# Kernel tuning notes

Measured on AMD Instinct MI355X. Metric: run time of the kernel, lower is better.

## Reference

```python
import jax, jax.numpy as jnp
import numpy as np

H = 8          # attention heads
EPS = 1e-5     # LayerNorm eps (torch default)
B, T, E = 8, 1024, 128
D, DI, N, DC, R = 512, 1024, 16, 4, 32   # d_model, d_inner, d_state, d_conv, dt_rank
NT, NM = 6, 8                            # transformer layers, mamba layers
FF = 2048                                # transformer dim_feedforward (torch default)


def setup_inputs():
    key = jax.random.key(0)
    ks = iter(jax.random.split(key, 48))
    def rn(shape, scale=0.05):
        return jax.random.normal(next(ks), shape, jnp.float32) * scale
    return {
        "emb":      jax.random.normal(next(ks), (B, T, E), jnp.float32),
        # TransformerEncoder (6 post-norm layers), params stacked on leading layer dim
        "t_wqkv":   rn((NT, 3 * E, E)), "t_bqkv": jnp.zeros((NT, 3 * E), jnp.float32),
        "t_wo":     rn((NT, E, E)),     "t_bo":   jnp.zeros((NT, E), jnp.float32),
        "t_ln1w":   jnp.ones((NT, E), jnp.float32),  "t_ln1b": jnp.zeros((NT, E), jnp.float32),
        "t_w1":     rn((NT, FF, E)),    "t_b1":   jnp.zeros((NT, FF), jnp.float32),
        "t_w2":     rn((NT, E, FF)),    "t_b2":   jnp.zeros((NT, E), jnp.float32),
        "t_ln2w":   jnp.ones((NT, E), jnp.float32),  "t_ln2b": jnp.zeros((NT, E), jnp.float32),
        # Linear(emb_dim -> d_model)
        "w_in":     rn((D, E)), "b_in": jnp.zeros((D,), jnp.float32),
        # MambaBlocks (8 raw Mamba layers, no residual/norm), stacked
        "m_inproj": rn((NM, 2 * DI, D)),
        "m_convw":  rn((NM, DI, DC), 0.2), "m_convb": jnp.zeros((NM, DI), jnp.float32),
        "m_xproj":  rn((NM, R + 2 * N, DI)),
        "m_dtw":    rn((NM, DI, R), 0.1),
        "m_dtb":    jax.random.uniform(next(ks), (NM, DI), jnp.float32, -6.0, -3.0),
        "m_Alog":   jnp.log(jnp.tile(jnp.arange(1, N + 1, dtype=jnp.float32), (NM, DI, 1))),
        "m_D":      jnp.ones((NM, DI), jnp.float32),
        "m_outproj": rn((NM, D, DI)),
        # Linear(d_model -> emb_dim)
        "w_out":    rn((E, D)), "b_out": jnp.zeros((E,), jnp.float32),
    }


def _ln(x, w, b):
    mu = jnp.mean(x, -1, keepdims=True)
    var = jnp.var(x, -1, keepdims=True)
    return (x - mu) * jax.lax.rsqrt(var + EPS) * w + b


def _tlayer(x, p):
    wqkv, bqkv, wo, bo, ln1w, ln1b, w1, b1, w2, b2, ln2w, ln2b = p
    qkv = x @ wqkv.T + bqkv                        # (B,T,3E)
    q, k, v = jnp.split(qkv, 3, axis=-1)
    def heads(t):                                  # (B,T,E) -> (B,H,T,E//H)
        return t.reshape(B, T, H, E // H).transpose(0, 2, 1, 3)
    q, k, v = heads(q), heads(k), heads(v)
    scores = jnp.einsum("bhqd,bhkd->bhqk", q, k) / jnp.sqrt(jnp.float32(E // H))
    attn = jax.nn.softmax(scores, axis=-1)
    o = jnp.einsum("bhqk,bhkd->bhqd", attn, v).transpose(0, 2, 1, 3).reshape(B, T, E)
    x = _ln(x + o @ wo.T + bo, ln1w, ln1b)         # post-norm (torch default)
    ff = jax.nn.relu(x @ w1.T + b1) @ w2.T + b2
    return _ln(x + ff, ln2w, ln2b)


def _mamba_layer(x, p):
    inproj, convw, convb, xproj, dtw, dtb, Alog, Dp, outproj = p
    xz = x @ inproj.T                              # (B,T,2*DI)
    xi, z = jnp.split(xz, 2, axis=-1)
    # causal depthwise conv1d, kernel DC, left-padded
    xp = jnp.pad(xi, ((0, 0), (DC - 1, 0), (0, 0)))
    conv = sum(xp[:, k:k + T, :] * convw[:, k] for k in range(DC)) + convb
    xi = jax.nn.silu(conv)
    dbc = xi @ xproj.T                             # (B,T,R+2N)
    dt_r, Bt, Ct = dbc[..., :R], dbc[..., R:R + N], dbc[..., R + N:]
    dt = jax.nn.softplus(dt_r @ dtw.T + dtb)       # (B,T,DI)
    A = -jnp.exp(Alog)                             # (DI,N)
    def step(h, inputs):
        dt_t, B_t, C_t, x_t = inputs               # (B,DI),(B,N),(B,N),(B,DI)
        dA = jnp.exp(dt_t[:, :, None] * A)         # (B,DI,N)
        h = h * dA + (dt_t * x_t)[:, :, None] * B_t[:, None, :]
        y = jnp.einsum("bdn,bn->bd", h, C_t)
        return h, y
    h0 = jnp.zeros((B, DI, N), x.dtype)
    seq = (dt.transpose(1, 0, 2), Bt.transpose(1, 0, 2),
           Ct.transpose(1, 0, 2), xi.transpose(1, 0, 2))
    _, ys = jax.lax.scan(step, h0, seq)            # ys: (T,B,DI)
    y = ys.transpose(1, 0, 2) + Dp * xi
    y = y * jax.nn.silu(z)
    return y @ outproj.T                           # (B,T,D)


def reference(emb, t_wqkv, t_bqkv, t_wo, t_bo, t_ln1w, t_ln1b, t_w1, t_b1, t_w2, t_b2,
              t_ln2w, t_ln2b, w_in, b_in, m_inproj, m_convw, m_convb, m_xproj, m_dtw,
              m_dtb, m_Alog, m_D, m_outproj, w_out, b_out):
    x = emb
    tparams = (t_wqkv, t_bqkv, t_wo, t_bo, t_ln1w, t_ln1b, t_w1, t_b1, t_w2, t_b2, t_ln2w, t_ln2b)
    for i in range(NT):
        x = _tlayer(x, tuple(p[i] for p in tparams))
    x = x @ w_in.T + b_in                          # (B,T,D)
    mparams = (m_inproj, m_convw, m_convb, m_xproj, m_dtw, m_dtb, m_Alog, m_D, m_outproj)
    for i in range(NM):
        x = _mamba_layer(x, tuple(p[i] for p in mparams))
    return x @ w_out.T + b_out                     # (B,T,E)
```

## Files before the change

### kernel.cpp

```cpp
#include <hip/hip_runtime.h>
#include <math.h>

#define HB 8
#define TT 1024
#define NSTATE 16
#define NTT 6
#define NMM 8
#define MM (HB*TT)
#define EPSV 1e-5f
#define CHUNK 64
#define NCH (TT/CHUNK)
#define LSTR 72
#define AKS 128
#define VSTR 132

typedef _Float16 f16x8 __attribute__((ext_vector_type(8)));
typedef _Float16 f16x4 __attribute__((ext_vector_type(4)));
typedef float f32x4_t __attribute__((ext_vector_type(4)));

static __device__ inline void split8(const float4 a, const float4 b,
                                     f16x8& h, f16x8& l)
{
  float x[8] = {a.x, a.y, a.z, a.w, b.x, b.y, b.z, b.w};
#pragma unroll
  for (int i = 0; i < 8; i++) {
    _Float16 hi = (_Float16)x[i];
    h[i] = hi;
    l[i] = (_Float16)(x[i] - (float)hi);
  }
}

template<int TN>
__global__ __launch_bounds__(256) void gemm_mfma_t(
    const float* __restrict__ A, int lda,
    const float* __restrict__ W,
    const float* __restrict__ bias,
    float* __restrict__ C,
    float* __restrict__ P,
    int N, int K, int S, int act)
{
  __shared__ _Float16 As[128 * LSTR];
  __shared__ _Float16 Bs[TN * LSTR];
  const int tid = threadIdx.x;
  const int m0 = blockIdx.y * 128;
  const int n0 = blockIdx.x * TN;
  const int z = blockIdx.z;
  const int kchunk = K / S;
  const int kb = z * kchunk;
  const int ke = kb + kchunk;

  const int lr = tid >> 1;
  const int lh = tid & 1;
  const int lane = tid & 63;
  const int w = tid >> 6;
  const int quad = lane >> 4;
  const int l16 = lane & 15;

  const float* Arow = A + (size_t)(m0 + lr) * lda + lh * 16;
  _Float16* Adst = &As[lr * LSTR + lh * 16];

  constexpr int MI = (TN == 128) ? 4 : 2;
  const int w0 = (TN == 128) ? (w & 1) : w;
  const int w1 = (TN == 128) ? (w >> 1) : 0;
  const int rowbase = (TN == 128) ? w0 * 64 : w0 * 32;

  f32x4_t acc[MI][4];
#pragma unroll
  for (int i = 0; i < MI; i++)
#pragma unroll
    for (int j = 0; j < 4; j++)
#pragma unroll
      for (int r = 0; r < 4; r++) acc[i][j][r] = 0.f;

  const _Float16* ab = &As[(rowbase + l16) * LSTR + quad * 8];
  const _Float16* bb = &Bs[(w1 * 64 + l16) * LSTR + quad * 8];

  const float* Wrow;
  _Float16* Bdst;
  if (TN == 128) {
    Wrow = W + (size_t)(n0 + lr) * K + lh * 16;
    Bdst = &Bs[lr * LSTR + lh * 16];
  } else {
    const int br = tid >> 2;
    const int bo = (tid & 3) * 8;
    Wrow = W + (size_t)(n0 + br) * K + bo;
    Bdst = &Bs[br * LSTR + bo];
  }

  for (int k0 = kb; k0 < ke; k0 += 32) {
    float4 a0 = *(const float4*)&Arow[k0];
    float4 a1 = *(const float4*)&Arow[k0 + 4];
    float4 a2 = *(const float4*)&Arow[k0 + 8];
    float4 a3 = *(const float4*)&Arow[k0 + 12];
    float4 b0 = *(const float4*)&Wrow[k0];
    float4 b1 = *(const float4*)&Wrow[k0 + 4];
    float4 b2, b3;
    if (TN == 128) {
      b2 = *(const float4*)&Wrow[k0 + 8];
      b3 = *(const float4*)&Wrow[k0 + 12];
    }
    __syncthreads();
    {
      f16x8 h, l;
      split8(a0, a1, h, l);
      *(f16x8*)&Adst[0] = h; *(f16x8*)&Adst[32] = l;
      split8(a2, a3, h, l);
      *(f16x8*)&Adst[8] = h; *(f16x8*)&Adst[40] = l;
      split8(b0, b1, h, l);
      *(f16x8*)&Bdst[0] = h; *(f16x8*)&Bdst[32] = l;
      if (TN == 128) {
        split8(b2, b3, h, l);
        *(f16x8*)&Bdst[8] = h; *(f16x8*)&Bdst[40] = l;
      }
    }
    __syncthreads();

    f16x8 bh[4], bl[4];
#pragma unroll
    for (int ni = 0; ni < 4; ni++) {
      bh[ni] = *(const f16x8*)&bb[ni * 16 * LSTR];
      bl[ni] = *(const f16x8*)&bb[ni * 16 * LSTR + 32];
    }
#pragma unroll
    for (int mi = 0; mi < MI; mi++) {
      f16x8 ah = *(const f16x8*)&ab[mi * 16 * LSTR];
      f16x8 al = *(const f16x8*)&ab[mi * 16 * LSTR + 32];
#pragma unroll
      for (int ni = 0; ni < 4; ni++) {
        acc[mi][ni] = __builtin_amdgcn_mfma_f32_16x16x32_f16(ah, bh[ni], acc[mi][ni], 0, 0, 0);
        acc[mi][ni] = __builtin_amdgcn_mfma_f32_16x16x32_f16(ah, bl[ni], acc[mi][ni], 0, 0, 0);
        acc[mi][ni] = __builtin_amdgcn_mfma_f32_16x16x32_f16(al, bh[ni], acc[mi][ni], 0, 0, 0);
      }
    }
  }

  float* dst = (S == 1) ? C : (P + (size_t)z * MM * N);
#pragma unroll
  for (int ni = 0; ni < 4; ni++) {
    const int n = n0 + w1 * 64 + ni * 16 + l16;
    const float bv = (S == 1 && bias) ? bias[n] : 0.f;
#pragma unroll
    for (int mi = 0; mi < MI; mi++) {
      const int mbase = m0 + rowbase + mi * 16 + quad * 4;
#pragma unroll
      for (int r = 0; r < 4; r++) {
        float v = acc[mi][ni][r] + bv;
        if (S == 1) {
          if (act == 1) v = fmaxf(v, 0.f);
          else if (act == 2) v = fmaxf(v, 0.f) + log1pf(__expf(-fabsf(v)));
        }
        dst[(size_t)(mbase + r) * N + n] = v;
      }
    }
  }
}

__global__ __launch_bounds__(256) void reduce_k(
    const float* __restrict__ P, const float* __restrict__ bias,
    float* __restrict__ C, int nmask, int S, int act, int stride4)
{
  const int idx = blockIdx.x * 256 + threadIdx.x;
  float4 a = *(const float4*)&P[(size_t)idx * 4];
  for (int z = 1; z < S; z++) {
    float4 p = *(const float4*)&P[(size_t)(idx + z * (size_t)stride4) * 4];
    a.x += p.x; a.y += p.y; a.z += p.z; a.w += p.w;
  }
  if (bias) {
    float4 bv = *(const float4*)&bias[(idx * 4) & nmask];
    a.x += bv.x; a.y += bv.y; a.z += bv.z; a.w += bv.w;
  }
  if (act == 1) {
    a.x = fmaxf(a.x, 0.f); a.y = fmaxf(a.y, 0.f);
    a.z = fmaxf(a.z, 0.f); a.w = fmaxf(a.w, 0.f);
  } else if (act == 2) {
    a.x = fmaxf(a.x, 0.f) + log1pf(__expf(-fabsf(a.x)));
    a.y = fmaxf(a.y, 0.f) + log1pf(__expf(-fabsf(a.y)));
    a.z = fmaxf(a.z, 0.f) + log1pf(__expf(-fabsf(a.z)));
    a.w = fmaxf(a.w, 0.f) + log1pf(__expf(-fabsf(a.w)));
  }
  *(float4*)&C[(size_t)idx * 4] = a;
}

__global__ __launch_bounds__(256) void attn_mfma_k(
    const float* __restrict__ qkv, float* __restrict__ o)
{
  __shared__ _Float16 Khi[AKS * 16], Klo[AKS * 16];
  __shared__ _Float16 Vthi[16 * VSTR], Vtlo[16 * VSTR];
  __shared__ float Pscr[4][16 * 18];

  const int tid = threadIdx.x;
  const int lane = tid & 63;
  const int wv = tid >> 6;
  const int quad = lane >> 4;
  const int l16 = lane & 15;
  const int qh = quad & 1;
  const int bh = blockIdx.y;
  const int b = bh >> 3;
  const int h = bh & 7;
  const int qb0 = blockIdx.x * 128;

  f16x8 qa[2];
#pragma unroll
  for (int u = 0; u < 2; u++) {
    const int qrow = qb0 + wv * 32 + u * 16 + l16;
    const float* qp = qkv + (size_t)(b * TT + qrow) * 384 + h * 16 + qh * 8;
    float4 x0 = *(const float4*)&qp[0];
    float4 x1 = *(const float4*)&qp[4];
    float xv[8] = {x0.x, x0.y, x0.z, x0.w, x1.x, x1.y, x1.z, x1.w};
#pragma unroll
    for (int j = 0; j < 8; j++) {
      float q = xv[j] * 0.25f;
      _Float16 hi = (_Float16)q;
      _Float16 lo = (_Float16)(q - (float)hi);
      qa[u][j] = (quad < 2) ? hi : lo;
    }
  }

  f32x4_t oacc[2];
  float lacc[2][4];
#pragma unroll
  for (int u = 0; u < 2; u++)
#pragma unroll
    for (int r = 0; r < 4; r++) { oacc[u][r] = 0.f; lacc[u][r] = 0.f; }

  float* Pw = &Pscr[wv][0];

  for (int ks = 0; ks < TT; ks += AKS) {
    __syncthreads();
    {
      const int key = tid >> 1, hf = tid & 1;
      const float* kp = qkv + (size_t)(b * TT + ks + key) * 384 + 128 + h * 16 + hf * 8;
      float4 k0 = *(const float4*)&kp[0];
      float4 k1 = *(const float4*)&kp[4];
      f16x8 vh, vl;
      split8(k0, k1, vh, vl);
      *(f16x8*)&Khi[key * 16 + hf * 8] = vh;
      *(f16x8*)&Klo[key * 16 + hf * 8] = vl;
      const float* vp = kp + 128;
      float4 v0 = *(const float4*)&vp[0];
      float4 v1 = *(const float4*)&vp[4];
      float vvv[8] = {v0.x, v0.y, v0.z, v0.w, v1.x, v1.y, v1.z, v1.w};
#pragma unroll
      for (int j = 0; j < 8; j++) {
        const int d = hf * 8 + j;
        _Float16 hi = (_Float16)vvv[j];
        Vthi[d * VSTR + key] = hi;
        Vtlo[d * VSTR + key] = (_Float16)(vvv[j] - (float)hi);
      }
    }
    __syncthreads();

    for (int kt = 0; kt < AKS; kt += 16) {
      f16x8 kfh = *(const f16x8*)&Khi[(kt + l16) * 16 + qh * 8];
      f16x8 kfl = *(const f16x8*)&Klo[(kt + l16) * 16 + qh * 8];
      const int vo = l16 * VSTR + kt + qh * 8;
      f16x4 va0 = *(const f16x4*)&Vthi[vo];
      f16x4 va1 = *(const f16x4*)&Vthi[vo + 4];
      f16x4 vb0 = *(const f16x4*)&Vtlo[vo];
      f16x4 vb1 = *(const f16x4*)&Vtlo[vo + 4];
      f16x8 vfh, vfl;
#pragma unroll
      for (int i = 0; i < 4; i++) {
        vfh[i] = va0[i]; vfh[4 + i] = va1[i];
        vfl[i] = vb0[i]; vfl[4 + i] = vb1[i];
      }

#pragma unroll
      for (int u = 0; u < 2; u++) {
        f32x4_t s;
#pragma unroll
        for (int r = 0; r < 4; r++) s[r] = 0.f;
        s = __builtin_amdgcn_mfma_f32_16x16x32_f16(qa[u], kfh, s, 0, 0, 0);
        s = __builtin_amdgcn_mfma_f32_16x16x32_f16(qa[u], kfl, s, 0, 0, 0);
        float p[4];
#pragma unroll
        for (int r = 0; r < 4; r++) {
          p[r] = __expf(s[r]);
          lacc[u][r] += p[r];
        }
        float* ps = Pw + (quad * 4) * 18 + l16;
        ps[0] = p[0]; ps[18] = p[1]; ps[36] = p[2]; ps[54] = p[3];
        __asm__ volatile("s_waitcnt lgkmcnt(0)" ::: "memory");
        const float* pr = Pw + l16 * 18 + qh * 8;
        f16x8 pa;
#pragma unroll
        for (int j = 0; j < 8; j++) {
          float pv = pr[j];
          _Float16 hi = (_Float16)pv;
          _Float16 lo = (_Float16)(pv - (float)hi);
          pa[j] = (quad < 2) ? hi : lo;
        }
        oacc[u] = __builtin_amdgcn_mfma_f32_16x16x32_f16(pa, vfh, oacc[u], 0, 0, 0);
        oacc[u] = __builtin_amdgcn_mfma_f32_16x16x32_f16(pa, vfl, oacc[u], 0, 0, 0);
        __asm__ volatile("s_waitcnt lgkmcnt(0)" ::: "memory");
      }
    }
  }

#pragma unroll
  for (int u = 0; u < 2; u++) {
#pragma unroll
    for (int r = 0; r < 4; r++) {
      float lv = lacc[u][r];
      lv += __shfl_xor(lv, 1);
      lv += __shfl_xor(lv, 2);
      lv += __shfl_xor(lv, 4);
      lv += __shfl_xor(lv, 8);
      const float inv = 1.f / lv;
      const int qrow = qb0 + wv * 32 + u * 16 + quad * 4 + r;
      o[(size_t)(b * TT + qrow) * 128 + h * 16 + l16] = oacc[u][r] * inv;
    }
  }
}

__global__ __launch_bounds__(256) void add_ln_k(
    const float* __restrict__ a, const float* __restrict__ bvec,
    const float* __restrict__ w, const float* __restrict__ bb,
    float* __restrict__ out)
{
  const int tid = threadIdx.x;
  const int wave = tid >> 6, lane = tid & 63;
  const size_t row = (size_t)blockIdx.x * 4 + wave;
  const float* pa = a + row * 128;
  const float* pb = bvec + row * 128;
  float v0 = pa[lane] + pb[lane];
  float v1 = pa[lane + 64] + pb[lane + 64];
  float s1 = v0 + v1, s2 = v0 * v0 + v1 * v1;
#pragma unroll
  for (int off = 32; off; off >>= 1) {
    s1 += __shfl_down(s1, off);
    s2 += __shfl_down(s2, off);
  }
  s1 = __shfl(s1, 0); s2 = __shfl(s2, 0);
  const float mean = s1 * (1.f / 128.f);
  const float var = s2 * (1.f / 128.f) - mean * mean;
  const float rs = rsqrtf(var + EPSV);
  out[row * 128 + lane]      = (v0 - mean) * rs * w[lane] + bb[lane];
  out[row * 128 + lane + 64] = (v1 - mean) * rs * w[lane + 64] + bb[lane + 64];
}

__global__ __launch_bounds__(256) void conv_silu_k(
    const float* __restrict__ xz, const float* __restrict__ cw,
    const float* __restrict__ cb, float* __restrict__ out)
{
  const int idx = blockIdx.x * 256 + threadIdx.x;
  const int di = idx & 1023;
  const int m = idx >> 10;
  const int t = m & (TT - 1);
  float acc = cb[di];
#pragma unroll
  for (int k = 0; k < 4; k++) {
    int tt = t + k - 3;
    if (tt >= 0) acc += xz[(size_t)(m + k - 3) * 2048 + di] * cw[di * 4 + k];
  }
  out[(size_t)m * 1024 + di] = acc / (1.f + __expf(-acc));
}

__global__ __launch_bounds__(64) void scan_partial_k(
    const float* __restrict__ dt,
    const float* __restrict__ dbc,
    const float* __restrict__ xi,
    const float* __restrict__ Alog,
    float* __restrict__ Pb, float* __restrict__ Sb)
{
  const int slice = blockIdx.x & 15;
  const int c = blockIdx.x >> 4;
  const int b = blockIdx.y;
  const int di = slice * 64 + threadIdx.x;

  float A[NSTATE];
#pragma unroll
  for (int n = 0; n < NSTATE; n++) A[n] = -__expf(Alog[di * NSTATE + n]);
  float h[NSTATE], P[NSTATE];
#pragma unroll
  for (int n = 0; n < NSTATE; n++) { h[n] = 0.f; P[n] = 1.f; }

  const size_t m0 = (size_t)b * TT + (size_t)c * CHUNK;
  for (int t = 0; t < CHUNK; t++) {
    const size_t m = m0 + t;
    const float dtv = dt[m * 1024 + di];
    const float xv  = xi[m * 1024 + di];
    const float dtx = dtv * xv;
#pragma unroll
    for (int n = 0; n < NSTATE; n++) {
      const float Bv = dbc[m * 64 + 32 + n];
      const float dA = __expf(dtv * A[n]);
      h[n] = h[n] * dA + dtx * Bv;
      P[n] *= dA;
    }
  }
  const size_t base = (((size_t)b * NCH + c) * NSTATE) * 1024 + di;
#pragma unroll
  for (int n = 0; n < NSTATE; n++) {
    Pb[base + (size_t)n * 1024] = P[n];
    Sb[base + (size_t)n * 1024] = h[n];
  }
}

__global__ __launch_bounds__(256) void scan_fix_k(
    float* __restrict__ Pb, const float* __restrict__ Sb)
{
  const int idx = blockIdx.x * 256 + threadIdx.x;
  const int b = idx >> 10;
  const int di = idx & 1023;
  float h[NSTATE];
#pragma unroll
  for (int n = 0; n < NSTATE; n++) h[n] = 0.f;
  for (int c = 0; c < NCH; c++) {
    const size_t base = (((size_t)b * NCH + c) * NSTATE) * 1024 + di;
    float P[NSTATE], S[NSTATE];
#pragma unroll
    for (int n = 0; n < NSTATE; n++) {
      P[n] = Pb[base + (size_t)n * 1024];
      S[n] = Sb[base + (size_t)n * 1024];
    }
#pragma unroll
    for (int n = 0; n < NSTATE; n++) {
      Pb[base + (size_t)n * 1024] = h[n];
      h[n] = P[n] * h[n] + S[n];
    }
  }
}

__global__ __launch_bounds__(64) void scan_final_k(
    const float* __restrict__ dt,
    const float* __restrict__ dbc,
    const float* __restrict__ xi,
    const float* __restrict__ xz,
    const float* __restrict__ Alog,
    const float* __restrict__ Dp,
    const float* __restrict__ Hin,
    float* __restrict__ Y)
{
  const int slice = blockIdx.x & 15;
  const int c = blockIdx.x >> 4;
  const int b = blockIdx.y;
  const int di = slice * 64 + threadIdx.x;

  float A[NSTATE];
#pragma unroll
  for (int n = 0; n < NSTATE; n++) A[n] = -__expf(Alog[di * NSTATE + n]);
  const float Dv = Dp[di];
  float h[NSTATE];
  const size_t hbase = (((size_t)b * NCH + c) * NSTATE) * 1024 + di;
#pragma unroll
  for (int n = 0; n < NSTATE; n++) h[n] = Hin[hbase + (size_t)n * 1024];

  const size_t m0 = (size_t)b * TT + (size_t)c * CHUNK;
  for (int t = 0; t < CHUNK; t++) {
    const size_t m = m0 + t;
    const float dtv = dt[m * 1024 + di];
    const float xv  = xi[m * 1024 + di];
    const float zv  = xz[m * 2048 + 1024 + di];
    const float dtx = dtv * xv;
    float y = 0.f;
#pragma unroll
    for (int n = 0; n < NSTATE; n++) {
      const float Bv = dbc[m * 64 + 32 + n];
      const float Cv = dbc[m * 64 + 48 + n];
      const float dA = __expf(dtv * A[n]);
      h[n] = h[n] * dA + dtx * Bv;
      y += h[n] * Cv;
    }
    y += Dv * xv;
    y *= zv / (1.f + __expf(-zv));
    Y[m * 1024 + di] = y;
  }
}

extern "C" void kernel_launch(void* const* d_in, const int* in_sizes, int n_in,
                              void* d_out, int out_size, void* d_ws, size_t ws_size,
                              hipStream_t stream)
{
  const float* emb      = (const float*)d_in[0];
  const float* t_wqkv   = (const float*)d_in[1];
  const float* t_bqkv   = (const float*)d_in[2];
  const float* t_wo     = (const float*)d_in[3];
  const float* t_bo     = (const float*)d_in[4];
  const float* t_ln1w   = (const float*)d_in[5];
  const float* t_ln1b   = (const float*)d_in[6];
  const float* t_w1     = (const float*)d_in[7];
  const float* t_b1     = (const float*)d_in[8];
  const float* t_w2     = (const float*)d_in[9];
  const float* t_b2     = (const float*)d_in[10];
  const float* t_ln2w   = (const float*)d_in[11];
  const float* t_ln2b   = (const float*)d_in[12];
  const float* w_in     = (const float*)d_in[13];
  const float* b_in     = (const float*)d_in[14];
  const float* m_inproj = (const float*)d_in[15];
  const float* m_convw  = (const float*)d_in[16];
  const float* m_convb  = (const float*)d_in[17];
  const float* m_xproj  = (const float*)d_in[18];
  const float* m_dtw    = (const float*)d_in[19];
  const float* m_dtb    = (const float*)d_in[20];
  const float* m_Alog   = (const float*)d_in[21];
  const float* m_D      = (const float*)d_in[22];
  const float* m_outproj= (const float*)d_in[23];
  const float* w_out    = (const float*)d_in[24];
  const float* b_out    = (const float*)d_in[25];

  float* ws = (float*)d_ws;
  float* X0   = ws;
  float* X1   = X0 + (size_t)MM * 512;
  float* Abuf = X1 + (size_t)MM * 512;
  float* Bf   = Abuf + (size_t)MM * 2048;
  float* Cf   = Bf + (size_t)MM * 1024;
  float* Yb   = Cf + (size_t)MM * 1024;
  float* Db   = Yb + (size_t)MM * 1024;

  dim3 blk(256);
  auto gemm = [&](const float* A, int lda, const float* W, const float* bias,
                  float* C, int N, int K, int act, int S, float* P, bool tn64) {
    dim3 g(N / (tn64 ? 64 : 128), MM / 128, S);
    if (tn64)
      hipLaunchKernelGGL(gemm_mfma_t<64>, g, blk, 0, stream,
                         A, lda, W, S == 1 ? bias : nullptr, C, P, N, K, S, act);
    else
      hipLaunchKernelGGL(gemm_mfma_t<128>, g, blk, 0, stream,
                         A, lda, W, S == 1 ? bias : nullptr, C, P, N, K, S, act);
    if (S > 1) {
      int stride4 = (MM * N) / 4;
      hipLaunchKernelGGL(reduce_k, dim3(stride4 / 256), blk, 0, stream,
                         P, bias, C, N - 1, S, act, stride4);
    }
  };

  const float* x = emb;
  for (int l = 0; l < NTT; l++) {
    gemm(x, 128, t_wqkv + (size_t)l * 384 * 128, t_bqkv + l * 384,
         Abuf, 384, 128, 0, 1, nullptr, false);
    hipLaunchKernelGGL(attn_mfma_k, dim3(TT / 128, HB * 8), blk, 0, stream,
                       Abuf, Yb);
    gemm(Yb, 128, t_wo + (size_t)l * 128 * 128, t_bo + l * 128,
         Cf, 128, 128, 0, 2, X1, true);
    hipLaunchKernelGGL(add_ln_k, dim3(MM / 4), blk, 0, stream,
                       x, Cf, t_ln1w + l * 128, t_ln1b + l * 128, X0);
    gemm(X0, 128, t_w1 + (size_t)l * 2048 * 128, t_b1 + l * 2048,
         Abuf, 2048, 128, 1, 1, nullptr, false);
    gemm(Abuf, 2048, t_w2 + (size_t)l * 128 * 2048, t_b2 + l * 128,
         Cf, 128, 2048, 0, 8, Yb, false);
    hipLaunchKernelGGL(add_ln_k, dim3(MM / 4), blk, 0, stream,
                       X0, Cf, t_ln2w + l * 128, t_ln2b + l * 128, X0);
    x = X0;
  }

  gemm(X0, 128, w_in, b_in, X1, 512, 128, 0, 1, nullptr, false);

  float* xc = X1;
  float* xo = X0;
  for (int l = 0; l < NMM; l++) {
    gemm(xc, 512, m_inproj + (size_t)l * 2048 * 512, nullptr,
         Abuf, 2048, 512, 0, 1, nullptr, false);
    hipLaunchKernelGGL(conv_silu_k, dim3(MM * 1024 / 256), blk, 0, stream,
                       Abuf, m_convw + (size_t)l * 1024 * 4, m_convb + l * 1024, Bf);
    gemm(Bf, 1024, m_xproj + (size_t)l * 64 * 1024, nullptr,
         Db, 64, 1024, 0, 4, xo, true);
    gemm(Db, 64, m_dtw + (size_t)l * 1024 * 32, m_dtb + l * 1024,
         Cf, 1024, 32, 2, 1, nullptr, false);

    float* Pb = xo;
    float* Sb = xo + (size_t)HB * NCH * NSTATE * 1024;
    hipLaunchKernelGGL(scan_partial_k, dim3(16 * NCH, HB), dim3(64), 0, stream,
                       Cf, Db, Bf, m_Alog + (size_t)l * 1024 * 16, Pb, Sb);
    hipLaunchKernelGGL(scan_fix_k, dim3(MM / 1024 * 4), blk, 0, stream, Pb, Sb);
    hipLaunchKernelGGL(scan_final_k, dim3(16 * NCH, HB), dim3(64), 0, stream,
                       Cf, Db, Bf, Abuf,
                       m_Alog + (size_t)l * 1024 * 16, m_D + l * 1024, Pb, Yb);

    gemm(Yb, 1024, m_outproj + (size_t)l * 512 * 1024, nullptr,
         xo, 512, 1024, 0, 2, Abuf, false);
    float* tmp = xc; xc = xo; xo = tmp;
  }

  gemm(xc, 512, w_out, b_out, (float*)d_out, 128, 512, 0, 4, Yb, false);
}
```

Before: 3.641 ms.

## Pre-split weights and GEMM activations into fp16 hi/lo planes before MFMA GEMMs

Adds a split kernel that converts fp32 tensors into separate fp16 high and low planes. All weight matrices are split once per forward call, and activations feeding the QKV, FF1, input-projection and Mamba in-projection GEMMs are split just before those GEMMs. The GEMM kernel can then load the pre-split fp16 planes straight into shared memory instead of converting fp32 to hi/lo in every tile, which each block otherwise repeats. The price is extra kernel launches, an extra pass over the split tensors, and a larger workspace. The weight pre-split path runs only when the workspace is big enough.

```diff
diff --git a/kernel.cpp b/kernel.cpp
--- a/kernel.cpp
+++ b/kernel.cpp
@@ -30,10 +30,30 @@
   }
 }
 
+__global__ __launch_bounds__(256) void split_k(
+    const float* __restrict__ X, _Float16* __restrict__ Hi,
+    _Float16* __restrict__ Lo)
+{
+  const size_t i = ((size_t)blockIdx.x * 256 + threadIdx.x) * 4;
+  float4 v = *(const float4*)&X[i];
+  float x[4] = {v.x, v.y, v.z, v.w};
+  f16x4 h, l;
+#pragma unroll
+  for (int j = 0; j < 4; j++) {
+    _Float16 hi = (_Float16)x[j];
+    h[j] = hi;
+    l[j] = (_Float16)(x[j] - (float)hi);
+  }
+  *(f16x4*)&Hi[i] = h;
+  *(f16x4*)&Lo[i] = l;
+}
+
 template<int TN>
 __global__ __launch_bounds__(256) void gemm_mfma_t(
     const float* __restrict__ A, int lda,
     const float* __restrict__ W,
+    const _Float16* __restrict__ Ahi, const _Float16* __restrict__ Alo,
+    const _Float16* __restrict__ Whi, const _Float16* __restrict__ Wlo,
     const float* __restrict__ bias,
     float* __restrict__ C,
     float* __restrict__ P,
@@ -57,6 +77,8 @@
   const int l16 = lane & 15;
 
   const float* Arow = A + (size_t)(m0 + lr) * lda + lh * 16;
+  const _Float16* AHrow = Ahi ? (Ahi + (size_t)(m0 + lr) * lda + lh * 16) : nullptr;
+  const _Float16* ALrow = Ahi ? (Alo + (size_t)(m0 + lr) * lda + lh * 16) : nullptr;
   _Float16* Adst = &As[lr * LSTR + lh * 16];
 
   constexpr int MI = (TN == 128) ? 4 : 2;
@@ -76,36 +98,74 @@
   const _Float16* bb = &Bs[(w1 * 64 + l16) * LSTR + quad * 8];
 
   const float* Wrow;
+  const _Float16* WHrow = nullptr;
+  const _Float16* WLrow = nullptr;
   _Float16* Bdst;
   if (TN == 128) {
     Wrow = W + (size_t)(n0 + lr) * K + lh * 16;
+    if (Whi) {
+      WHrow = Whi + (size_t)(n0 + lr) * K + lh * 16;
+      WLrow = Wlo + (size_t)(n0 + lr) * K + lh * 16;
+    }
     Bdst = &Bs[lr * LSTR + lh * 16];
   } else {
     const int br = tid >> 2;
     const int bo = (tid & 3) * 8;
     Wrow = W + (size_t)(n0 + br) * K + bo;
+    if (Whi) {
+      WHrow = Whi + (size_t)(n0 + br) * K + bo;
+      WLrow = Wlo + (size_t)(n0 + br) * K + bo;
+    }
     Bdst = &Bs[br * LSTR + bo];
   }
 
   for (int k0 = kb; k0 < ke; k0 += 32) {
-    float4 a0 = *(const float4*)&Arow[k0];
-    float4 a1 = *(const float4*)&Arow[k0 + 4];
-    float4 a2 = *(const float4*)&Arow[k0 + 8];
-    float4 a3 = *(const float4*)&Arow[k0 + 12];
-    float4 b0 = *(const float4*)&Wrow[k0];
-    float4 b1 = *(const float4*)&Wrow[k0 + 4];
-    float4 b2, b3;
-    if (TN == 128) {
-      b2 = *(const float4*)&Wrow[k0 + 8];
-      b3 = *(const float4*)&Wrow[k0 + 12];
+    f16x8 ah0, ah1, al0, al1;
+    float4 a0, a1, a2, a3;
+    if (Ahi) {
+      ah0 = *(const f16x8*)&AHrow[k0];
+      ah1 = *(const f16x8*)&AHrow[k0 + 8];
+      al0 = *(const f16x8*)&ALrow[k0];
+      al1 = *(const f16x8*)&ALrow[k0 + 8];
+    } else {
+      a0 = *(const float4*)&Arow[k0];
+      a1 = *(const float4*)&Arow[k0 + 4];
+      a2 = *(const float4*)&Arow[k0 + 8];
+      a3 = *(const float4*)&Arow[k0 + 12];
+    }
+    f16x8 wh0, wh1, wl0, wl1;
+    float4 b0, b1, b2, b3;
+    if (Whi) {
+      wh0 = *(const f16x8*)&WHrow[k0];
+      wl0 = *(const f16x8*)&WLrow[k0];
+      if (TN == 128) {
+        wh1 = *(const f16x8*)&WHrow[k0 + 8];
+        wl1 = *(const f16x8*)&WLrow[k0 + 8];
+      }
+    } else {
+      b0 = *(const float4*)&Wrow[k0];
+      b1 = *(const float4*)&Wrow[k0 + 4];
+      if (TN == 128) {
+        b2 = *(const float4*)&Wrow[k0 + 8];
+        b3 = *(const float4*)&Wrow[k0 + 12];
+      }
     }
     __syncthreads();
-    {
+    if (Ahi) {
+      *(f16x8*)&Adst[0] = ah0; *(f16x8*)&Adst[8] = ah1;
+      *(f16x8*)&Adst[32] = al0; *(f16x8*)&Adst[40] = al1;
+    } else {
       f16x8 h, l;
       split8(a0, a1, h, l);
       *(f16x8*)&Adst[0] = h; *(f16x8*)&Adst[32] = l;
       split8(a2, a3, h, l);
       *(f16x8*)&Adst[8] = h; *(f16x8*)&Adst[40] = l;
+    }
+    if (Whi) {
+      *(f16x8*)&Bdst[0] = wh0; *(f16x8*)&Bdst[32] = wl0;
+      if (TN == 128) { *(f16x8*)&Bdst[8] = wh1; *(f16x8*)&Bdst[40] = wl1; }
+    } else {
+      f16x8 h, l;
       split8(b0, b1, h, l);
       *(f16x8*)&Bdst[0] = h; *(f16x8*)&Bdst[32] = l;
       if (TN == 128) {
@@ -123,13 +183,13 @@
     }
 #pragma unroll
     for (int mi = 0; mi < MI; mi++) {
-      f16x8 ah = *(const f16x8*)&ab[mi * 16 * LSTR];
-      f16x8 al = *(const f16x8*)&ab[mi * 16 * LSTR + 32];
+      f16x8 fah = *(const f16x8*)&ab[mi * 16 * LSTR];
+      f16x8 fal = *(const f16x8*)&ab[mi * 16 * LSTR + 32];
 #pragma unroll
       for (int ni = 0; ni < 4; ni++) {
-        acc[mi][ni] = __builtin_amdgcn_mfma_f32_16x16x32_f16(ah, bh[ni], acc[mi][ni], 0, 0, 0);
-        acc[mi][ni] = __builtin_amdgcn_mfma_f32_16x16x32_f16(ah, bl[ni], acc[mi][ni], 0, 0, 0);
-        acc[mi][ni] = __builtin_amdgcn_mfma_f32_16x16x32_f16(al, bh[ni], acc[mi][ni], 0, 0, 0);
+        acc[mi][ni] = __builtin_amdgcn_mfma_f32_16x16x32_f16(fah, bh[ni], acc[mi][ni], 0, 0, 0);
+        acc[mi][ni] = __builtin_amdgcn_mfma_f32_16x16x32_f16(fah, bl[ni], acc[mi][ni], 0, 0, 0);
+        acc[mi][ni] = __builtin_amdgcn_mfma_f32_16x16x32_f16(fal, bh[ni], acc[mi][ni], 0, 0, 0);
       }
     }
   }
@@ -508,16 +568,56 @@
   float* Yb   = Cf + (size_t)MM * 1024;
   float* Db   = Yb + (size_t)MM * 1024;
 
+  const size_t baseFloats = (size_t)MM * 6208;
+  const size_t wqE = (size_t)NTT * 384 * 128;
+  const size_t woE = (size_t)NTT * 128 * 128;
+  const size_t w1E = (size_t)NTT * 2048 * 128;
+  const size_t w2E = (size_t)NTT * 128 * 2048;
+  const size_t wiE = (size_t)512 * 128;
+  const size_t ipE = (size_t)NMM * 2048 * 512;
+  const size_t xpE = (size_t)NMM * 64 * 1024;
+  const size_t dwE = (size_t)NMM * 1024 * 32;
+  const size_t opE = (size_t)NMM * 512 * 1024;
+  const size_t woutE = (size_t)128 * 512;
+  const size_t totalWE = wqE + woE + w1E + w2E + wiE + ipE + xpE + dwE + opE + woutE;
+  const bool pre = ws_size >= baseFloats * 4 + totalWE * 4;
+  _Float16* Wa = (_Float16*)(ws + baseFloats);
+  size_t off = 0;
+  auto plane = [&](size_t cnt) { _Float16* p = Wa + off; off += 2 * cnt; return p; };
+  _Float16* wqP = plane(wqE); _Float16* woP = plane(woE);
+  _Float16* w1P = plane(w1E); _Float16* w2P = plane(w2E);
+  _Float16* wiP = plane(wiE); _Float16* ipP = plane(ipE);
+  _Float16* xpP = plane(xpE); _Float16* dwP = plane(dwE);
+  _Float16* opP = plane(opE); _Float16* woutP = plane(woutE);
+
   dim3 blk(256);
+  auto dosplit = [&](const float* src, _Float16* hi, size_t cnt) {
+    hipLaunchKernelGGL(split_k, dim3((unsigned)(cnt / 1024)), blk, 0, stream,
+                       src, hi, hi + cnt);
+  };
+  if (pre) {
+    dosplit(t_wqkv, wqP, wqE);   dosplit(t_wo, woP, woE);
+    dosplit(t_w1, w1P, w1E);     dosplit(t_w2, w2P, w2E);
+    dosplit(w_in, wiP, wiE);     dosplit(m_inproj, ipP, ipE);
+    dosplit(m_xproj, xpP, xpE);  dosplit(m_dtw, dwP, dwE);
+    dosplit(m_outproj, opP, opE); dosplit(w_out, woutP, woutE);
+  }
+
   auto gemm = [&](const float* A, int lda, const float* W, const float* bias,
-                  float* C, int N, int K, int act, int S, float* P, bool tn64) {
+                  float* C, int N, int K, int act, int S, float* P, bool tn64,
+                  const _Float16* Ahi, const _Float16* Whi, size_t wcnt) {
     dim3 g(N / (tn64 ? 64 : 128), MM / 128, S);
+    const _Float16* Alo = Ahi ? Ahi + (size_t)MM * K : nullptr;
+    const _Float16* Wlo = (pre && Whi) ? Whi + wcnt : nullptr;
+    const _Float16* Whi2 = pre ? Whi : nullptr;
     if (tn64)
       hipLaunchKernelGGL(gemm_mfma_t<64>, g, blk, 0, stream,
-                         A, lda, W, S == 1 ? bias : nullptr, C, P, N, K, S, act);
+                         A, lda, W, Ahi, Alo, Whi2, Wlo,
+                         S == 1 ? bias : nullptr, C, P, N, K, S, act);
     else
       hipLaunchKernelGGL(gemm_mfma_t<128>, g, blk, 0, stream,
-                         A, lda, W, S == 1 ? bias : nullptr, C, P, N, K, S, act);
+                         A, lda, W, Ahi, Alo, Whi2, Wlo,
+                         S == 1 ? bias : nullptr, C, P, N, K, S, act);
     if (S > 1) {
       int stride4 = (MM * N) / 4;
       hipLaunchKernelGGL(reduce_k, dim3(stride4 / 256), blk, 0, stream,
@@ -527,36 +627,58 @@
 
   const float* x = emb;
   for (int l = 0; l < NTT; l++) {
+    _Float16* aP = (_Float16*)Cf;
+    hipLaunchKernelGGL(split_k, dim3(MM * 128 / 1024), blk, 0, stream,
+                       x, aP, aP + (size_t)MM * 128);
     gemm(x, 128, t_wqkv + (size_t)l * 384 * 128, t_bqkv + l * 384,
-         Abuf, 384, 128, 0, 1, nullptr, false);
+         Abuf, 384, 128, 0, 1, nullptr, false,
+         aP, wqP + (size_t)l * 384 * 128, wqE);
     hipLaunchKernelGGL(attn_mfma_k, dim3(TT / 128, HB * 8), blk, 0, stream,
                        Abuf, Yb);
     gemm(Yb, 128, t_wo + (size_t)l * 128 * 128, t_bo + l * 128,
-         Cf, 128, 128, 0, 2, X1, true);
+         Cf, 128, 128, 0, 2, X1, true,
+         nullptr, woP + (size_t)l * 128 * 128, woE);
     hipLaunchKernelGGL(add_ln_k, dim3(MM / 4), blk, 0, stream,
                        x, Cf, t_ln1w + l * 128, t_ln1b + l * 128, X0);
+    aP = (_Float16*)Yb;
+    hipLaunchKernelGGL(split_k, dim3(MM * 128 / 1024), blk, 0, stream,
+                       X0, aP, aP + (size_t)MM * 128);
     gemm(X0, 128, t_w1 + (size_t)l * 2048 * 128, t_b1 + l * 2048,
-         Abuf, 2048, 128, 1, 1, nullptr, false);
+         Abuf, 2048, 128, 1, 1, nullptr, false,
+         aP, w1P + (size_t)l * 2048 * 128, w1E);
     gemm(Abuf, 2048, t_w2 + (size_t)l * 128 * 2048, t_b2 + l * 128,
-         Cf, 128, 2048, 0, 8, Yb, false);
+         Cf, 128, 2048, 0, 8, Yb, false,
+         nullptr, w2P + (size_t)l * 128 * 2048, w2E);
     hipLaunchKernelGGL(add_ln_k, dim3(MM / 4), blk, 0, stream,
                        X0, Cf, t_ln2w + l * 128, t_ln2b + l * 128, X0);
     x = X0;
   }
 
-  gemm(X0, 128, w_in, b_in, X1, 512, 128, 0, 1, nullptr, false);
+  {
+    _Float16* aP = (_Float16*)Cf;
+    hipLaunchKernelGGL(split_k, dim3(MM * 128 / 1024), blk, 0, stream,
+                       X0, aP, aP + (size_t)MM * 128);
+    gemm(X0, 128, w_in, b_in, X1, 512, 128, 0, 1, nullptr, false,
+         aP, wiP, wiE);
+  }
 
   float* xc = X1;
   float* xo = X0;
   for (int l = 0; l < NMM; l++) {
+    _Float16* aP = (_Float16*)Cf;
+    hipLaunchKernelGGL(split_k, dim3(MM * 512 / 1024), blk, 0, stream,
+                       xc, aP, aP + (size_t)MM * 512);
     gemm(xc, 512, m_inproj + (size_t)l * 2048 * 512, nullptr,
-         Abuf, 2048, 512, 0, 1, nullptr, false);
+         Abuf, 2048, 512, 0, 1, nullptr, false,
+         aP, ipP + (size_t)l * 2048 * 512, ipE);
     hipLaunchKernelGGL(conv_silu_k, dim3(MM * 1024 / 256), blk, 0, stream,
                        Abuf, m_convw + (size_t)l * 1024 * 4, m_convb + l * 1024, Bf);
     gemm(Bf, 1024, m_xproj + (size_t)l * 64 * 1024, nullptr,
-         Db, 64, 1024, 0, 4, xo, true);
+         Db, 64, 1024, 0, 4, xo, true,
+         nullptr, xpP + (size_t)l * 64 * 1024, xpE);
     gemm(Db, 64, m_dtw + (size_t)l * 1024 * 32, m_dtb + l * 1024,
-         Cf, 1024, 32, 2, 1, nullptr, false);
+         Cf, 1024, 32, 2, 1, nullptr, false,
+         nullptr, dwP + (size_t)l * 1024 * 32, dwE);
 
     float* Pb = xo;
     float* Sb = xo + (size_t)HB * NCH * NSTATE * 1024;
@@ -568,9 +690,11 @@
                        m_Alog + (size_t)l * 1024 * 16, m_D + l * 1024, Pb, Yb);
 
     gemm(Yb, 1024, m_outproj + (size_t)l * 512 * 1024, nullptr,
-         xo, 512, 1024, 0, 2, Abuf, false);
+         xo, 512, 1024, 0, 2, Abuf, false,
+         nullptr, opP + (size_t)l * 512 * 1024, opE);
     float* tmp = xc; xc = xo; xo = tmp;
   }
 
-  gemm(xc, 512, w_out, b_out, (float*)d_out, 128, 512, 0, 4, Yb, false);
-}
+  gemm(xc, 512, w_out, b_out, (float*)d_out, 128, 512, 0, 4, Yb, false,
+       nullptr, woutP, woutE);
+}
```

After: 3.783 ms. 3.9% more time.
